# Kernel optimization log

Measured on AMD Instinct MI355X. Metric: run time of the kernel, lower is better.

## Reference

```python
import jax, jax.numpy as jnp
import numpy as np

# Fixed module configuration (matches init_kwargs)
B, T, H, W, C = 2, 16, 32, 32, 512
NH, DH = 8, 64          # num_heads, head_dim = C // NH
MLP = 2048
EPS = 1e-6              # flax LayerNorm default epsilon


def _xavier(key, shape):
    fan_in, fan_out = shape[-2], shape[-1]
    lim = np.sqrt(6.0 / (fan_in + fan_out)).astype(np.float32)
    return jax.random.uniform(key, shape, jnp.float32, -lim, lim)


def setup_inputs() -> dict:
    key = jax.random.key(0)
    ks = jax.random.split(key, 8)
    return {
        "x": jax.random.normal(ks[0], (B, T * H * W, C), jnp.float32),
        # per-axis (stacked: 0=time, 1=height, 2=width) attention params
        "ln_scale": jnp.ones((3, C), jnp.float32),
        "ln_bias": jnp.zeros((3, C), jnp.float32),
        "wq": _xavier(ks[1], (3, C, C)), "bq": jnp.zeros((3, C), jnp.float32),
        "wk": _xavier(ks[2], (3, C, C)), "bk": jnp.zeros((3, C), jnp.float32),
        "wv": _xavier(ks[3], (3, C, C)), "bv": jnp.zeros((3, C), jnp.float32),
        "wo": _xavier(ks[4], (3, C, C)), "bo": jnp.zeros((3, C), jnp.float32),
        # final LN + MLP params
        "ln_mlp_scale": jnp.ones((C,), jnp.float32),
        "ln_mlp_bias": jnp.zeros((C,), jnp.float32),
        "w1": _xavier(ks[5], (C, MLP)),
        "b1": jax.random.normal(ks[6], (MLP,), jnp.float32) * 1e-6,
        "w2": _xavier(ks[7], (MLP, C)),
        "b2": jnp.zeros((C,), jnp.float32),
    }


def _ln(x, scale, bias):
    m = jnp.mean(x, axis=-1, keepdims=True)
    v = jnp.var(x, axis=-1, keepdims=True)
    return (x - m) * jax.lax.rsqrt(v + EPS) * scale + bias


def _mha(x, wq, bq, wk, bk, wv, bv, wo, bo):
    # x: [Bf, S, C]; standard flax-style MHA (query scaled by 1/sqrt(head_dim))
    Bf, S, _ = x.shape
    q = (x @ wq + bq).reshape(Bf, S, NH, DH) * (1.0 / np.sqrt(DH).astype(np.float32))
    k = (x @ wk + bk).reshape(Bf, S, NH, DH)
    v = (x @ wv + bv).reshape(Bf, S, NH, DH)
    a = jax.nn.softmax(jnp.einsum('bqhd,bkhd->bhqk', q, k), axis=-1)
    o = jnp.einsum('bhqk,bkhd->bqhd', a, v).reshape(Bf, S, C)
    return o @ wo + bo


def _axial(x5, axis, sc, bi, wq, bq, wk, bk, wv, bv, wo, bo):
    # fold all non-`axis` spatial dims into batch, attend along `axis`
    other = [a for a in (1, 2, 3) if a != axis]
    perm = [0] + other + [axis, 4]
    xp = jnp.transpose(x5, perm)                      # [..., S_axis, C]
    pshape = xp.shape
    x1 = xp.reshape(-1, pshape[-2], C)                # [Bf, S_axis, C]
    y = _mha(_ln(x1, sc, bi), wq, bq, wk, bk, wv, bv, wo, bo) + x1  # pre-LN residual
    y = y.reshape(pshape)
    inv = list(np.argsort(perm))
    return jnp.transpose(y, inv)


def reference(x, ln_scale, ln_bias, wq, bq, wk, bk, wv, bv, wo, bo,
              ln_mlp_scale, ln_mlp_bias, w1, b1, w2, b2):
    x5 = x.reshape(B, T, H, W, C)
    for i, axis in enumerate((1, 2, 3)):  # time, height, width
        x5 = _axial(x5, axis, ln_scale[i], ln_bias[i], wq[i], bq[i],
                    wk[i], bk[i], wv[i], bv[i], wo[i], bo[i])
    xf = x5.reshape(B, T * H * W, C)
    y = _ln(xf, ln_mlp_scale, ln_mlp_bias)
    y = jax.nn.gelu(y @ w1 + b1) @ w2 + b2            # gelu approximate=True (flax default)
    return xf + y
```

## Files before the change

### kernel.cpp

```cpp
#include <hip/hip_runtime.h>
#include <hip/hip_bf16.h>

typedef __attribute__((ext_vector_type(8))) short short8;
typedef __attribute__((ext_vector_type(4))) float f32x4;

static __device__ __forceinline__ short f2bf(float f) {
    union { __hip_bfloat16 h; short s; } u;
    u.h = __float2bfloat16(f);
    return u.s;
}

static __device__ __forceinline__ float gelu_tanh(float v) {
    const float c = 0.7978845608028654f;
    float t = tanhf(c * (v + 0.044715f * v * v * v));
    return 0.5f * v * (1.f + t);
}

static __device__ __forceinline__ void gload16(const void* g, void* l) {
    __builtin_amdgcn_global_load_lds(
        (const __attribute__((address_space(1))) void*)g,
        (__attribute__((address_space(3))) void*)l, 16, 0, 0);
}

__global__ __launch_bounds__(256) void cvt_weights(
    const float* __restrict__ wq, const float* __restrict__ wk,
    const float* __restrict__ wv, const float* __restrict__ wo,
    const float* __restrict__ w1, const float* __restrict__ w2,
    short* __restrict__ wT)
{
    const long NSQ = 12L * 262144;
    long gid = (long)blockIdx.x * 256 + threadIdx.x;
    if (gid < NSQ) {
        int m = (int)(gid >> 18);
        int rem = (int)(gid & 262143);
        int n = rem >> 9, k = rem & 511;
        int a = m >> 2, t = m & 3;
        const float* src = (t == 0) ? wq : (t == 1) ? wk : (t == 2) ? wv : wo;
        wT[gid] = f2bf(src[(long)a * 262144 + (long)k * 512 + n]);
    } else if (gid < NSQ + 1048576) {
        int r = (int)(gid - NSQ);
        int n = r >> 9, k = r & 511;
        wT[gid] = f2bf(w1[(long)k * 2048 + n]);
    } else {
        int r = (int)(gid - NSQ - 1048576);
        int n = r >> 11, k = r & 2047;
        wT[gid] = f2bf(w2[(long)k * 512 + n]);
    }
}

__global__ __launch_bounds__(256) void ln_kernel(
    const float* __restrict__ x, const float* __restrict__ sc,
    const float* __restrict__ bi, short* __restrict__ out)
{
    int row = blockIdx.x * 4 + (threadIdx.x >> 6);
    int lane = threadIdx.x & 63;
    const float* xr = x + (long)row * 512 + lane * 8;
    f32x4 v0 = *(const f32x4*)xr;
    f32x4 v1 = *(const f32x4*)(xr + 4);
    float s = 0.f, ss = 0.f;
#pragma unroll
    for (int i = 0; i < 4; i++) { s += v0[i] + v1[i]; ss += v0[i] * v0[i] + v1[i] * v1[i]; }
#pragma unroll
    for (int m = 1; m < 64; m <<= 1) { s += __shfl_xor(s, m, 64); ss += __shfl_xor(ss, m, 64); }
    float mean = s * (1.f / 512.f);
    float var  = ss * (1.f / 512.f) - mean * mean;
    float rs = rsqrtf(var + 1e-6f);
    f32x4 s0 = *(const f32x4*)(sc + lane * 8);
    f32x4 s1 = *(const f32x4*)(sc + lane * 8 + 4);
    f32x4 b0 = *(const f32x4*)(bi + lane * 8);
    f32x4 b1 = *(const f32x4*)(bi + lane * 8 + 4);
    short8 o;
#pragma unroll
    for (int i = 0; i < 4; i++) o[i]     = f2bf((v0[i] - mean) * rs * s0[i] + b0[i]);
#pragma unroll
    for (int i = 0; i < 4; i++) o[4 + i] = f2bf((v1[i] - mean) * rs * s1[i] + b1[i]);
    *(short8*)(out + (long)row * 512 + lane * 8) = o;
}

template<int EPI>
__global__ __launch_bounds__(256, 2) void gemm_nt(
    const short* __restrict__ A, const short* __restrict__ Bt,
    const float* __restrict__ bias, const float* __restrict__ bias2,
    const float* __restrict__ bias3,
    const float* __restrict__ res, float* __restrict__ outf,
    short* __restrict__ outb, int M, int N, int K, float scale)
{
    __shared__ __align__(16) short As[128 * 64];
    __shared__ __align__(16) short Bs[128 * 64];
    const int t = threadIdx.x;
    const int lane = t & 63, wid = t >> 6;
    const int wm = wid >> 1, wn = wid & 1;

    const int nbx = gridDim.x;
    const int bid = blockIdx.y * nbx + blockIdx.x;
    const int q8 = (nbx * gridDim.y) >> 3;
    const int swz = (bid & 7) * q8 + (bid >> 3);
    const int m0 = (swz % nbx) * 128, n0 = (swz / nbx) * 128;

    const short* Ag = A  + (long)m0 * K;
    const short* Bg = Bt + (long)n0 * K;

    f32x4 acc[4][4];
#pragma unroll
    for (int i = 0; i < 4; i++)
#pragma unroll
        for (int j = 0; j < 4; j++) acc[i][j] = (f32x4){0.f, 0.f, 0.f, 0.f};

    const long rowOff = (long)(t >> 3) * K + (t & 7) * 8;
    const int  ldsOff = t * 16;
    const int NT = K >> 6;

    for (int tt = 0; tt < NT; ++tt) {
        const short* Asrc = Ag + tt * 64 + rowOff;
        const short* Bsrc = Bg + tt * 64 + rowOff;
#pragma unroll
        for (int c = 0; c < 4; c++) {
            gload16(Asrc + (long)c * 32 * K, (char*)As + c * 4096 + ldsOff);
            gload16(Bsrc + (long)c * 32 * K, (char*)Bs + c * 4096 + ldsOff);
        }
        __syncthreads();

        const int arow = wm * 64 + (lane & 15);
        const int brow = wn * 64 + (lane & 15);
        const int kb = (lane >> 4) * 16;
#pragma unroll
        for (int ks = 0; ks < 2; ++ks) {
            short8 af[4], bfr[4];
#pragma unroll
            for (int f = 0; f < 4; f++) {
                af[f]  = *(short8*)((char*)As + (arow + f * 16) * 128 + kb + ks * 64);
                bfr[f] = *(short8*)((char*)Bs + (brow + f * 16) * 128 + kb + ks * 64);
            }
#pragma unroll
            for (int i = 0; i < 4; i++)
#pragma unroll
                for (int j = 0; j < 4; j++)
                    acc[i][j] = __builtin_amdgcn_mfma_f32_16x16x32_bf16(af[i], bfr[j], acc[i][j], 0, 0, 0);
        }
        __syncthreads();
    }

#pragma unroll
    for (int j = 0; j < 4; j++) {
        int col = n0 + wn * 64 + j * 16 + (lane & 15);
        float bv;
        float sc_part = 1.f;
        if (EPI == 3) {
            int part = col >> 9;
            const float* bp = (part == 0) ? bias : (part == 1) ? bias2 : bias3;
            bv = bp[col & 511];
            if (part == 0) sc_part = scale;
        } else {
            bv = bias[col];
        }
#pragma unroll
        for (int i = 0; i < 4; i++) {
            int row0 = m0 + wm * 64 + i * 16 + ((lane >> 4) << 2);
#pragma unroll
            for (int r = 0; r < 4; r++) {
                int row = row0 + r;
                long idx = (long)row * N + col;
                float v = acc[i][j][r] + bv;
                if (EPI == 1)      outf[idx] = v + res[idx];
                else if (EPI == 2) outb[idx] = f2bf(gelu_tanh(v));
                else               outb[idx] = f2bf(v * sc_part);
            }
        }
    }
}

template<int S, int PASS>
__global__ __launch_bounds__(64) void attn_kernel(
    const short* __restrict__ Q, const short* __restrict__ Kx,
    const short* __restrict__ V, short* __restrict__ O, int ld)
{
    constexpr int MF = S / 16;
    constexpr int SP = 32;
    __shared__ __align__(16) short P_lds[S * SP];
    __shared__ __align__(16) short Vt[64 * SP];

    const int lane = threadIdx.x;
    const int pair = blockIdx.x;
    const int head = pair & 7;
    const int bf = pair >> 3;
    long base; int stride;
    if (PASS == 0)      { base = (long)(bf >> 10) * 16384 + (bf & 1023); stride = 1024; }
    else if (PASS == 1) { int b = bf >> 9, t = (bf >> 5) & 15, w = bf & 31; base = (long)b * 16384 + t * 1024 + w; stride = 32; }
    else                { int b = bf >> 9, t = (bf >> 5) & 15, h = bf & 31; base = (long)b * 16384 + t * 1024 + (h << 5); stride = 1; }
    const int hoff = head * 64;

    if (S == 16) {
        short8 z = {0, 0, 0, 0, 0, 0, 0, 0};
        *(short8*)(P_lds + lane * 8) = z;
#pragma unroll
        for (int i = 0; i < 4; i++) *(short8*)(Vt + lane * 32 + i * 8) = z;
        __syncthreads();
    }

    short8 qf[MF][2], kf[MF][2];
#pragma unroll
    for (int f = 0; f < MF; f++) {
        int r = f * 16 + (lane & 15);
        const short* qp = Q + (base + (long)r * stride) * ld + hoff + ((lane >> 4) * 8);
        qf[f][0] = *(const short8*)qp;
        qf[f][1] = *(const short8*)(qp + 32);
        const short* kp = Kx + (base + (long)r * stride) * ld + hoff + ((lane >> 4) * 8);
        kf[f][0] = *(const short8*)kp;
        kf[f][1] = *(const short8*)(kp + 32);
    }

    short8 vv[4];
    const int vr  = (S == 32) ? (lane & 31) : (lane & 15);
    const int vd0 = (S == 32) ? ((lane >> 5) * 32) : ((lane >> 4) * 16);
    constexpr int NVC = (S == 32) ? 4 : 2;
    {
        const short* vp = V + (base + (long)vr * stride) * ld + hoff + vd0;
#pragma unroll
        for (int c = 0; c < NVC; c++) vv[c] = *(const short8*)(vp + c * 8);
    }
#pragma unroll
    for (int c = 0; c < NVC; c++)
#pragma unroll
        for (int e = 0; e < 8; e++)
            Vt[(vd0 + c * 8 + e) * SP + vr] = vv[c][e];

    f32x4 zero4 = {0.f, 0.f, 0.f, 0.f};
    f32x4 sc[MF][MF];
#pragma unroll
    for (int i = 0; i < MF; i++)
#pragma unroll
        for (int j = 0; j < MF; j++) {
            f32x4 a = __builtin_amdgcn_mfma_f32_16x16x32_bf16(qf[i][0], kf[j][0], zero4, 0, 0, 0);
            sc[i][j] = __builtin_amdgcn_mfma_f32_16x16x32_bf16(qf[i][1], kf[j][1], a, 0, 0, 0);
        }

#pragma unroll
    for (int i = 0; i < MF; i++) {
#pragma unroll
        for (int r = 0; r < 4; r++) {
            float mx = sc[i][0][r];
            if (MF == 2) mx = fmaxf(mx, sc[i][1][r]);
#pragma unroll
            for (int m = 1; m < 16; m <<= 1) mx = fmaxf(mx, __shfl_xor(mx, m, 64));
            float e0 = expf(sc[i][0][r] - mx);
            float e1 = (MF == 2) ? expf(sc[i][1][r] - mx) : 0.f;
            float sum = e0 + e1;
#pragma unroll
            for (int m = 1; m < 16; m <<= 1) sum += __shfl_xor(sum, m, 64);
            float inv = 1.f / sum;
            int row = i * 16 + ((lane >> 4) << 2) + r;
            P_lds[row * SP + (lane & 15)] = f2bf(e0 * inv);
            if (MF == 2) P_lds[row * SP + 16 + (lane & 15)] = f2bf(e1 * inv);
        }
    }
    __syncthreads();

    short8 pa[MF];
#pragma unroll
    for (int f = 0; f < MF; f++)
        pa[f] = *(const short8*)(P_lds + (f * 16 + (lane & 15)) * SP + (lane >> 4) * 8);
    short8 vbf[4];
#pragma unroll
    for (int n = 0; n < 4; n++)
        vbf[n] = *(const short8*)(Vt + (n * 16 + (lane & 15)) * SP + (lane >> 4) * 8);
    f32x4 of[MF][4];
#pragma unroll
    for (int f = 0; f < MF; f++)
#pragma unroll
        for (int n = 0; n < 4; n++)
            of[f][n] = __builtin_amdgcn_mfma_f32_16x16x32_bf16(pa[f], vbf[n], zero4, 0, 0, 0);

#pragma unroll
    for (int f = 0; f < MF; f++) {
        int q0 = f * 16 + ((lane >> 4) << 2);
#pragma unroll
        for (int n = 0; n < 4; n++) {
            int d = n * 16 + (lane & 15);
#pragma unroll
            for (int r = 0; r < 4; r++)
                O[(base + (long)(q0 + r) * stride) * 512 + hoff + d] = f2bf(of[f][n][r]);
        }
    }
}

extern "C" void kernel_launch(void* const* d_in, const int* in_sizes, int n_in,
                              void* d_out, int out_size, void* d_ws, size_t ws_size,
                              hipStream_t stream)
{
    const float* x   = (const float*)d_in[0];
    const float* lns = (const float*)d_in[1];
    const float* lnb = (const float*)d_in[2];
    const float* wq  = (const float*)d_in[3];
    const float* bq  = (const float*)d_in[4];
    const float* wk  = (const float*)d_in[5];
    const float* bk  = (const float*)d_in[6];
    const float* wv  = (const float*)d_in[7];
    const float* bv  = (const float*)d_in[8];
    const float* wo  = (const float*)d_in[9];
    const float* bo  = (const float*)d_in[10];
    const float* lms = (const float*)d_in[11];
    const float* lmb = (const float*)d_in[12];
    const float* w1  = (const float*)d_in[13];
    const float* b1  = (const float*)d_in[14];
    const float* w2  = (const float*)d_in[15];
    const float* b2  = (const float*)d_in[16];

    char* ws = (char*)d_ws;
    short* wT   = (short*)ws;
    short* bufA = (short*)(ws + 10485760);
    short* big  = (short*)(ws + 10485760 + 33554432);
    float* xcur = (float*)d_out;

    const int M = 32768;

    cvt_weights<<<20480, 256, 0, stream>>>(wq, wk, wv, wo, w1, w2, wT);

    for (int p = 0; p < 3; ++p) {
        const float* xin = (p == 0) ? x : xcur;
        ln_kernel<<<8192, 256, 0, stream>>>(xin, lns + p * 512, lnb + p * 512, bufA);
        const short* wqkvT = wT + (long)(p * 4) * 262144;
        const short* woT   = wT + (long)(p * 4 + 3) * 262144;
        gemm_nt<3><<<dim3(256, 12), 256, 0, stream>>>(bufA, wqkvT,
            bq + p * 512, bk + p * 512, bv + p * 512,
            nullptr, nullptr, big, M, 1536, 512, 0.125f);
        const short* qb = big, *kb = big + 512, *vbp = big + 1024;
        if (p == 0)      attn_kernel<16, 0><<<16384, 64, 0, stream>>>(qb, kb, vbp, bufA, 1536);
        else if (p == 1) attn_kernel<32, 1><<<8192, 64, 0, stream>>>(qb, kb, vbp, bufA, 1536);
        else             attn_kernel<32, 2><<<8192, 64, 0, stream>>>(qb, kb, vbp, bufA, 1536);
        gemm_nt<1><<<dim3(256, 4), 256, 0, stream>>>(bufA, woT,
            bo + p * 512, nullptr, nullptr, xin, xcur, nullptr, M, 512, 512, 1.f);
    }

    ln_kernel<<<8192, 256, 0, stream>>>(xcur, lms, lmb, bufA);
    const short* w1T = wT + 12L * 262144;
    const short* w2T = wT + 12L * 262144 + 1048576;
    gemm_nt<2><<<dim3(256, 16), 256, 0, stream>>>(bufA, w1T, b1,
        nullptr, nullptr, nullptr, nullptr, big, M, 2048, 512, 1.f);
    gemm_nt<1><<<dim3(256, 4), 256, 0, stream>>>(big, w2T, b2,
        nullptr, nullptr, xcur, xcur, nullptr, M, 512, 2048, 1.f);
}
```

Before: 1.073 ms.

## Stage bf16 GEMM epilogue through LDS for vectorized stores; drop block swizzle

For the bf16-output GEMM epilogues (QKV projection and GELU MLP), accumulators are written to a swizzled LDS tile and then read back so each lane emits 16-byte row-contiguous bf16 stores instead of scattered 2-byte stores. This targets the write-coalescing inefficiency of the MFMA fragment layout. The change also removes the grouped block-index swizzle in favour of plain blockIdx mapping, which may reduce L2 reuse of A/B tiles. The staging adds two extra barriers and LDS traffic per tile.

```diff
diff --git a/kernel.cpp b/kernel.cpp
--- a/kernel.cpp
+++ b/kernel.cpp
@@ -90,12 +90,7 @@
     const int t = threadIdx.x;
     const int lane = t & 63, wid = t >> 6;
     const int wm = wid >> 1, wn = wid & 1;
-
-    const int nbx = gridDim.x;
-    const int bid = blockIdx.y * nbx + blockIdx.x;
-    const int q8 = (nbx * gridDim.y) >> 3;
-    const int swz = (bid & 7) * q8 + (bid >> 3);
-    const int m0 = (swz % nbx) * 128, n0 = (swz / nbx) * 128;
+    const int m0 = blockIdx.x * 128, n0 = blockIdx.y * 128;
 
     const short* Ag = A  + (long)m0 * K;
     const short* Bg = Bt + (long)n0 * K;
@@ -140,31 +135,65 @@
         __syncthreads();
     }
 
-#pragma unroll
-    for (int j = 0; j < 4; j++) {
-        int col = n0 + wn * 64 + j * 16 + (lane & 15);
-        float bv;
-        float sc_part = 1.f;
-        if (EPI == 3) {
-            int part = col >> 9;
-            const float* bp = (part == 0) ? bias : (part == 1) ? bias2 : bias3;
-            bv = bp[col & 511];
-            if (part == 0) sc_part = scale;
-        } else {
-            bv = bias[col];
-        }
-#pragma unroll
-        for (int i = 0; i < 4; i++) {
-            int row0 = m0 + wm * 64 + i * 16 + ((lane >> 4) << 2);
-#pragma unroll
-            for (int r = 0; r < 4; r++) {
-                int row = row0 + r;
-                long idx = (long)row * N + col;
-                float v = acc[i][j][r] + bv;
-                if (EPI == 1)      outf[idx] = v + res[idx];
-                else if (EPI == 2) outb[idx] = f2bf(gelu_tanh(v));
-                else               outb[idx] = f2bf(v * sc_part);
+    if (EPI == 1) {
+#pragma unroll
+        for (int j = 0; j < 4; j++) {
+            int col = n0 + wn * 64 + j * 16 + (lane & 15);
+            float bv = bias[col];
+#pragma unroll
+            for (int i = 0; i < 4; i++) {
+                int row0 = m0 + wm * 64 + i * 16 + ((lane >> 4) << 2);
+#pragma unroll
+                for (int r = 0; r < 4; r++) {
+                    long idx = (long)(row0 + r) * N + col;
+                    outf[idx] = acc[i][j][r] + bv + res[idx];
+                }
             }
+        }
+    } else {
+        float* sl = (float*)(wid < 2 ? (void*)As : (void*)Bs) + (wid & 1) * 2048;
+        const int r0g = m0 + wm * 64;
+        const int c0g = n0 + wn * 64;
+#pragma unroll
+        for (int half = 0; half < 2; ++half) {
+#pragma unroll
+            for (int jj = 0; jj < 2; ++jj) {
+                int j = half * 2 + jj;
+                int col = c0g + j * 16 + (lane & 15);
+                float bv, sc_part = 1.f;
+                if (EPI == 3) {
+                    int part = col >> 9;
+                    const float* bp = (part == 0) ? bias : (part == 1) ? bias2 : bias3;
+                    bv = bp[col & 511];
+                    if (part == 0) sc_part = scale;
+                } else {
+                    bv = bias[col];
+                }
+#pragma unroll
+                for (int i = 0; i < 4; i++)
+#pragma unroll
+                    for (int r = 0; r < 4; r++) {
+                        int rl = i * 16 + ((lane >> 4) << 2) + r;
+                        int cl = jj * 16 + (lane & 15);
+                        float v = (acc[i][j][r] + bv) * sc_part;
+                        if (EPI == 2) v = gelu_tanh(v);
+                        sl[(rl * 32 + cl) ^ ((rl & 7) << 2)] = v;
+                    }
+            }
+            __syncthreads();
+#pragma unroll
+            for (int s = 0; s < 4; s++) {
+                int rl = s * 16 + (lane >> 2);
+                int fb = rl * 32 + (lane & 3) * 8;
+                int sw = (rl & 7) << 2;
+                f32x4 lo = *(f32x4*)&sl[fb ^ sw];
+                f32x4 hi = *(f32x4*)&sl[(fb + 4) ^ sw];
+                short8 o;
+#pragma unroll
+                for (int e = 0; e < 4; e++) { o[e] = f2bf(lo[e]); o[4 + e] = f2bf(hi[e]); }
+                *(short8*)(outb + (long)(r0g + rl) * N + c0g + half * 32 + (lane & 3) * 8) = o;
+            }
+            if (half == 0) __syncthreads();
         }
     }
 }
```

Result: slower. 1.103 ms (+2.8%).
